# Kernel tuning notes

Hardware: AMD Instinct MI355X
Metric: run time of the kernel (lower is better)

Reference implementation:

```python
import jax, jax.numpy as jnp
import numpy as np

B, S, L, E, H, T, V, D = 32, 256, 24, 300, 256, 16, 50000, 256  # batch, sents, words/sent, emb, gru_units, topics, vocab, dense


def setup_inputs() -> dict:
    key = jax.random.key(0)
    ks = jax.random.split(key, 12)
    word_ids = jax.random.randint(ks[0], (B, S, L), 0, V, dtype=jnp.int32)
    tsize = S // T
    starts = (jnp.arange(T, dtype=jnp.int32) * tsize + 1)          # 1-indexed inclusive
    ends = (jnp.arange(T, dtype=jnp.int32) * tsize + tsize)
    topic_start_ends = jnp.broadcast_to(jnp.stack([starts, ends], -1)[None], (B, T, 2))
    g = lambda k, shape, sc=0.05: (jax.random.normal(k, shape, jnp.float32) * sc)
    return {
        "word_ids": word_ids,
        "topic_start_ends": topic_start_ends,
        "emb": g(ks[1], (V, E), 0.1),
        "Wih_f": g(ks[2], (3 * H, E)), "Whh_f": g(ks[3], (3 * H, H)),
        "bih_f": jnp.zeros((3 * H,), jnp.float32), "bhh_f": jnp.zeros((3 * H,), jnp.float32),
        "Wih_b": g(ks[4], (3 * H, E)), "Whh_b": g(ks[5], (3 * H, H)),
        "bih_b": jnp.zeros((3 * H,), jnp.float32), "bhh_b": jnp.zeros((3 * H,), jnp.float32),
        "W_att": g(ks[6], (4 * H, 4 * H)), "v_att": g(ks[7], (4 * H, 1)),
        "W_dna": g(ks[8], (4 * H, D)), "b_dna": jnp.zeros((D,), jnp.float32),
        "W_out": g(ks[9], (D, 1)), "b_out": jnp.zeros((1,), jnp.float32),
    }


def _gru_dir(x, Wih, Whh, bih, bhh, reverse):
    # x: [B, S, E] -> outputs [B, S, H], final hidden [B, H]  (PyTorch GRU cell math)
    def step(h, xt):
        gi = xt @ Wih.T + bih
        gh = h @ Whh.T + bhh
        ir, iz, inn = jnp.split(gi, 3, axis=-1)
        hr, hz, hn = jnp.split(gh, 3, axis=-1)
        r = jax.nn.sigmoid(ir + hr)
        z = jax.nn.sigmoid(iz + hz)
        n = jnp.tanh(inn + r * hn)
        h2 = (1.0 - z) * n + z * h
        return h2, h2
    h0 = jnp.zeros((x.shape[0], Whh.shape[1]), x.dtype)
    hT, ys = jax.lax.scan(step, h0, jnp.swapaxes(x, 0, 1), reverse=reverse)
    return jnp.swapaxes(ys, 0, 1), hT


def _gather_seq(x, idx):
    # x: [B, S', C], idx: [B, K] -> [B, K, C]
    return jnp.take_along_axis(x, idx[:, :, None].astype(jnp.int32), axis=1)


def reference(word_ids, topic_start_ends, emb, Wih_f, Whh_f, bih_f, bhh_f,
              Wih_b, Whh_b, bih_b, bhh_b, W_att, v_att, W_dna, b_dna, W_out, b_out):
    # --- sent_encoder: per-sentence mean of word embeddings ---
    sent_vecs = jnp.mean(emb[word_ids], axis=2)  # [B, S, E]

    # --- doc_encoder: bidirectional GRU ---
    out_f, hT_f = _gru_dir(sent_vecs, Wih_f, Whh_f, bih_f, bhh_f, reverse=False)
    out_b, hT_b = _gru_dir(sent_vecs, Wih_b, Whh_b, bih_b, bhh_b, reverse=True)
    sent_rep = jnp.concatenate([out_f, out_b], axis=-1)          # [B, S, 2H]
    hidden = jnp.stack([hT_f, hT_b], axis=0)                     # [2, B, H]
    # faithful to torch: hidden.view(batch_size, 2H) (row-major reshape)
    doc_vec = hidden.reshape(B, 2 * H)
    doc_rep = jnp.broadcast_to(doc_vec[:, None, :], (B, S, 2 * H))

    # --- topic representation via boundary differencing on front/back-padded output ---
    padded = jnp.pad(sent_rep, ((0, 0), (1, 1), (0, 0)))         # [B, S+2, 2H]
    starts = topic_start_ends[..., 0]                            # [B, T], 1-indexed
    ends = topic_start_ends[..., 1]
    topic_fwd = _gather_seq(padded, ends)[..., :H] - _gather_seq(padded, starts - 1)[..., :H]
    topic_bwd = _gather_seq(padded, starts)[..., H:] - _gather_seq(padded, ends + 1)[..., H:]
    topic_mat = jnp.concatenate([topic_fwd, topic_bwd], axis=-1)  # [B, T, 2H]
    # sentence s (0-indexed) -> topic t with starts[t] <= s+1 <= ends[t]
    sent_1idx = jnp.arange(1, S + 1, dtype=jnp.int32)
    topic_id = jax.vmap(lambda e: jnp.searchsorted(e, sent_1idx, side='left'))(ends)  # [B, S]
    topic_rep = jnp.take_along_axis(topic_mat, topic_id[:, :, None], axis=1)          # [B, S, 2H]

    # --- decoder_attention ---
    cat_ds = jnp.concatenate([doc_rep, sent_rep], axis=-1)       # [B, S, 4H]
    cat_ts = jnp.concatenate([topic_rep, sent_rep], axis=-1)
    doc_scores = jnp.tanh(cat_ds @ W_att) @ v_att                # [B, S, 1]
    topic_scores = jnp.tanh(cat_ts @ W_att) @ v_att
    doc_w = jax.nn.softmax(doc_scores, axis=1)
    topic_w = jax.nn.softmax(topic_scores, axis=1)
    context = doc_w * doc_rep + topic_w * topic_rep              # [B, S, 2H]
    inp = jnp.concatenate([sent_rep, context], axis=-1)          # [B, S, 4H]
    h = jax.nn.relu(inp @ W_dna + b_dna)                         # dropout is identity (eval)
    logits = (h @ W_out + b_out)[..., 0]                         # [B, S]
    return logits
```

## Files before the change

### kernel.cpp

```cpp
#include <hip/hip_runtime.h>
#include <hip/hip_bf16.h>
#include <math.h>

#define Bd 32
#define Sd 256
#define Ld 24
#define Ed 300
#define Hd 256
#define Td 16
#define Dd 256
#define EP 320

using short8 = __attribute__((ext_vector_type(8))) short;
using f32x4  = __attribute__((ext_vector_type(4))) float;

__device__ __forceinline__ float fsigm(float x) { return 1.f / (1.f + __expf(-x)); }
__device__ __forceinline__ float ftanh(float x) {
  float e = __expf(2.f * x);
  return 1.f - 2.f / (e + 1.f);
}

__global__ void sent_means_kernel(const int* __restrict__ wids,
                                  const float* __restrict__ emb,
                                  __hip_bfloat16* __restrict__ apad) {
  int r = blockIdx.x;
  __shared__ int ids[Ld];
  int tid = threadIdx.x;
  if (tid < Ld) ids[tid] = wids[r * Ld + tid];
  __syncthreads();
  float acc = 0.f;
  if (tid < Ed) {
#pragma unroll
    for (int w = 0; w < Ld; ++w) acc += emb[(size_t)ids[w] * Ed + tid];
    acc *= (1.f / 24.f);
  }
  apad[r * EP + tid] = __float2bfloat16(tid < Ed ? acc : 0.f);
}

__global__ void pad_wih_kernel(const float* __restrict__ src,
                               __hip_bfloat16* __restrict__ dst) {
  int i = blockIdx.x * 256 + threadIdx.x;
  if (i >= 768 * EP) return;
  int n = i / EP, k = i % EP;
  dst[i] = __float2bfloat16(k < Ed ? src[n * Ed + k] : 0.f);
}
__global__ void f2bf_kernel(const float* __restrict__ src,
                            __hip_bfloat16* __restrict__ dst, int n) {
  int i = blockIdx.x * 256 + threadIdx.x;
  if (i < n) dst[i] = __float2bfloat16(src[i]);
}
__global__ void transpose_att_kernel(const float* __restrict__ src,
                                     __hip_bfloat16* __restrict__ dst) {
  int i = blockIdx.x * 256 + threadIdx.x;
  int n = i >> 10, k = i & 1023;
  dst[i] = __float2bfloat16(src[k * 1024 + n]);
}
__global__ void transpose_dna_kernel(const float* __restrict__ src,
                                     __hip_bfloat16* __restrict__ dst) {
  int i = blockIdx.x * 256 + threadIdx.x;
  int n = i >> 10, k = i & 1023;
  dst[i] = __float2bfloat16(src[k * Dd + n]);
}

__global__ __launch_bounds__(256) void gemm_xwt_kernel(
    const __hip_bfloat16* __restrict__ A, int lda,
    const __hip_bfloat16* __restrict__ W, int ldw,
    float* __restrict__ C, int ldc,
    int M, int N, int K,
    const float* __restrict__ bias) {
  __shared__ unsigned short la[64][32];
  __shared__ unsigned short lb[64][32];
  const int tid = threadIdx.x;
  const int m0 = blockIdx.x * 64, n0 = blockIdx.y * 64;
  const int lane = tid & 63, wid = tid >> 6;
  const int wm = (wid >> 1) * 32, wn = (wid & 1) * 32;
  const int lrow = tid >> 2, lcol = (tid & 3) * 8;
  f32x4 acc00 = {0.f, 0.f, 0.f, 0.f}, acc01 = {0.f, 0.f, 0.f, 0.f};
  f32x4 acc10 = {0.f, 0.f, 0.f, 0.f}, acc11 = {0.f, 0.f, 0.f, 0.f};
  int arow = m0 + lrow; if (arow > M - 1) arow = M - 1;
  const int brow = n0 + lrow;
  const int fr = lane & 15, fq = (lane >> 4) * 8;
  for (int k0 = 0; k0 < K; k0 += 32) {
    uint4 av = *(const uint4*)(A + (size_t)arow * lda + k0 + lcol);
    uint4 bv = *(const uint4*)(W + (size_t)brow * ldw + k0 + lcol);
    *(uint4*)(&la[lrow][lcol]) = av;
    *(uint4*)(&lb[lrow][lcol]) = bv;
    __syncthreads();
    short8 a0 = *(const short8*)(&la[wm + fr][fq]);
    short8 a1 = *(const short8*)(&la[wm + 16 + fr][fq]);
    short8 b0 = *(const short8*)(&lb[wn + fr][fq]);
    short8 b1 = *(const short8*)(&lb[wn + 16 + fr][fq]);
    acc00 = __builtin_amdgcn_mfma_f32_16x16x32_bf16(a0, b0, acc00, 0, 0, 0);
    acc01 = __builtin_amdgcn_mfma_f32_16x16x32_bf16(a0, b1, acc01, 0, 0, 0);
    acc10 = __builtin_amdgcn_mfma_f32_16x16x32_bf16(a1, b0, acc10, 0, 0, 0);
    acc11 = __builtin_amdgcn_mfma_f32_16x16x32_bf16(a1, b1, acc11, 0, 0, 0);
    __syncthreads();
  }
  const int rq = (lane >> 4) * 4;
  f32x4 accs[2][2] = {{acc00, acc01}, {acc10, acc11}};
  for (int i = 0; i < 2; ++i)
    for (int j = 0; j < 2; ++j) {
      int n = n0 + wn + j * 16 + fr;
      float bv = bias ? bias[n] : 0.f;
      for (int r2 = 0; r2 < 4; ++r2) {
        int m = m0 + wm + i * 16 + rq + r2;
        if (m < M) C[(size_t)m * ldc + n] = accs[i][j][r2] + bv;
      }
    }
}

__global__ __launch_bounds__(512, 2) void gru_mfma_kernel(
    const float* __restrict__ gi_f, const float* __restrict__ gi_b,
    const __hip_bfloat16* __restrict__ whhbf_f, const __hip_bfloat16* __restrict__ whhbf_b,
    const float* __restrict__ bhh_f, const float* __restrict__ bhh_b,
    float* __restrict__ sent_rep, __hip_bfloat16* __restrict__ sent_rep_bf,
    float* __restrict__ hT_f, float* __restrict__ hT_b) {
  __shared__ float gi_lds[2][8][768];
  __shared__ __hip_bfloat16 h_bf[256];
  __shared__ float gh[768];
  __shared__ float stg32[8][256];
  const int blk = blockIdx.x;
  const int dir = blk >> 5, b = blk & 31;
  const int tid = threadIdx.x;
  const int lane = tid & 63, w = tid >> 6;
  const float* gi = dir ? gi_b : gi_f;
  const __hip_bfloat16* whh = dir ? whhbf_b : whhbf_f;
  const float* bhh = dir ? bhh_b : bhh_f;

  if (tid < 256) h_bf[tid] = __float2bfloat16(0.f);

  short8 bfrag[6][8];
  {
    const int n0 = w * 96 + (lane & 15);
    const int kq = (lane >> 4) * 8;
#pragma unroll
    for (int nt = 0; nt < 6; ++nt)
#pragma unroll
      for (int kt = 0; kt < 8; ++kt)
        bfrag[nt][kt] = *(const short8*)(whh + (size_t)(n0 + nt * 16) * 256 + kt * 32 + kq);
  }
  float bhr = 0.f, bhz = 0.f, bhn = 0.f, hprev = 0.f;
  if (tid < 256) { bhr = bhh[tid]; bhz = bhh[256 + tid]; bhn = bhh[512 + tid]; }

  auto burst = [&](int tstart, int buf) {
#pragma unroll
    for (int i = 0; i < 3; ++i) {
      int idx = tid + i * 512;
      int u = idx / 192;
      int c4 = (idx - u * 192) * 4;
      int s = dir ? (255 - (tstart + u)) : (tstart + u);
      float4 v = *(const float4*)(gi + (size_t)(((b << 8) + s) * 768 + c4));
      *(float4*)(&gi_lds[buf][u][c4]) = v;
    }
  };
  burst(0, 0);
  __syncthreads();

  const int c = lane & 15;
  const int kq = (lane >> 4) * 8;
  const short8 zero8 = {0, 0, 0, 0, 0, 0, 0, 0};

  for (int t = 0; t < Sd; ++t) {
    if ((t & 7) == 0 && t + 8 < Sd) burst(t + 8, ((t >> 3) + 1) & 1);
    f32x4 acc[6];
#pragma unroll
    for (int nt = 0; nt < 6; ++nt) acc[nt] = (f32x4){0.f, 0.f, 0.f, 0.f};
#pragma unroll
    for (int kt = 0; kt < 8; ++kt) {
      short8 av = *(const short8*)(&h_bf[kt * 32 + kq]);
      if (c != 0) av = zero8;
#pragma unroll
      for (int nt = 0; nt < 6; ++nt)
        acc[nt] = __builtin_amdgcn_mfma_f32_16x16x32_bf16(av, bfrag[nt][kt], acc[nt], 0, 0, 0);
    }
    if (lane < 16) {
#pragma unroll
      for (int nt = 0; nt < 6; ++nt)
        gh[w * 96 + nt * 16 + lane] = acc[nt][0];
    }
    __syncthreads();
    if (tid < 256) {
      const float* gl = gi_lds[(t >> 3) & 1][t & 7];
      float rr = fsigm(gl[tid] + gh[tid] + bhr);
      float zz = fsigm(gl[256 + tid] + gh[256 + tid] + bhz);
      float nn = ftanh(gl[512 + tid] + rr * (gh[512 + tid] + bhn));
      float hn = (1.f - zz) * nn + zz * hprev;
      hprev = hn;
      h_bf[tid] = __float2bfloat16(hn);
      stg32[t & 7][tid] = hn;
    }
    __syncthreads();
    if ((t & 7) == 7) {
      const int base = t - 7;
#pragma unroll
      for (int i = 0; i < 4; ++i) {
        int idx = tid + i * 512;
        int u = idx >> 8, d = idx & 255;
        int sg = dir ? (255 - (base + u)) : (base + u);
        size_t rowg = (size_t)((b << 8) + sg);
        int col = dir ? (256 + d) : d;
        float v = stg32[u][d];
        sent_rep[rowg * 512 + col] = v;
        sent_rep_bf[rowg * 512 + col] = __float2bfloat16(v);
      }
    }
  }
  if (tid < 256) (dir ? hT_b : hT_f)[b * 256 + tid] = hprev;
}

__global__ void docvec_kernel(const float* __restrict__ hTf, const float* __restrict__ hTb,
                              __hip_bfloat16* __restrict__ dv) {
  int b = blockIdx.x, jj = threadIdx.x;
  int idx = b * 512 + jj;
  int dsel = idx >> 13;
  int rem = idx & 8191;
  int bp = rem >> 8, hp = rem & 255;
  float v = (dsel ? hTb : hTf)[bp * Hd + hp];
  dv[idx] = __float2bfloat16(v);
}

__global__ void topic_kernel(const int* __restrict__ tse, const float* __restrict__ sent_rep,
                             __hip_bfloat16* __restrict__ topic_bf) {
  int bt = blockIdx.x;
  int b = bt >> 4;
  int st = tse[bt * 2], en = tse[bt * 2 + 1];
  int dd = threadIdx.x;
  auto pad = [&](int i, int col) -> float {
    if (i < 1 || i > Sd) return 0.f;
    return sent_rep[((size_t)((b << 8) + (i - 1))) * 512 + col];
  };
  float fwd = pad(en, dd) - pad(st - 1, dd);
  float bwd = pad(st, Hd + dd) - pad(en + 1, Hd + dd);
  topic_bf[(size_t)bt * 512 + dd] = __float2bfloat16(fwd);
  topic_bf[(size_t)bt * 512 + Hd + dd] = __float2bfloat16(bwd);
}

__global__ void scores_kernel(const float* __restrict__ P, const float* __restrict__ R,
                              const float* __restrict__ Q, const float* __restrict__ v_att,
                              const int* __restrict__ tse,
                              float* __restrict__ dsc, float* __restrict__ tsc) {
  int r = blockIdx.x;
  int b = r >> 8, s = r & 255;
  int tid = threadIdx.x;
  int tsel = Td - 1;
  for (int t = 0; t < Td; ++t) {
    if (tse[(b * Td + t) * 2 + 1] >= s + 1) { tsel = t; break; }
  }
  const float* q = Q + (size_t)r * 1024;
  const float* p = P + (size_t)b * 1024;
  const float* rr = R + (size_t)(b * Td + tsel) * 1024;
  float accd = 0.f, acct = 0.f;
  for (int n = tid; n < 1024; n += 256) {
    float qv = q[n];
    float vv = v_att[n];
    accd += ftanh(p[n] + qv) * vv;
    acct += ftanh(rr[n] + qv) * vv;
  }
  __shared__ float s1[256], s2[256];
  s1[tid] = accd; s2[tid] = acct;
  __syncthreads();
  for (int off = 128; off > 0; off >>= 1) {
    if (tid < off) { s1[tid] += s1[tid + off]; s2[tid] += s2[tid + off]; }
    __syncthreads();
  }
  if (tid == 0) { dsc[r] = s1[0]; tsc[r] = s2[0]; }
}

__global__ void softmax_kernel(const float* __restrict__ dsc, const float* __restrict__ tsc,
                               float* __restrict__ dw, float* __restrict__ tw) {
  int b = blockIdx.x, s = threadIdx.x;
  __shared__ float red[256];
  for (int which = 0; which < 2; ++which) {
    const float* src = which ? tsc : dsc;
    float v = src[b * Sd + s];
    red[s] = v; __syncthreads();
    for (int off = 128; off > 0; off >>= 1) {
      if (s < off) red[s] = fmaxf(red[s], red[s + off]);
      __syncthreads();
    }
    float m = red[0]; __syncthreads();
    float e = __expf(v - m);
    red[s] = e; __syncthreads();
    for (int off = 128; off > 0; off >>= 1) {
      if (s < off) red[s] += red[s + off];
      __syncthreads();
    }
    float sum = red[0]; __syncthreads();
    (which ? tw : dw)[b * Sd + s] = e / sum;
  }
}

__global__ void final_kernel(const float* __restrict__ U, const float* __restrict__ dvd,
                             const float* __restrict__ tvd, const float* __restrict__ dw,
                             const float* __restrict__ tw, const float* __restrict__ b_dna,
                             const float* __restrict__ w_out,
                             const float* __restrict__ b_out,
                             const int* __restrict__ tse, float* __restrict__ out) {
  int r = blockIdx.x;
  int b = r >> 8, s = r & 255;
  int dd = threadIdx.x;
  int tsel = Td - 1;
  for (int t = 0; t < Td; ++t) {
    if (tse[(b * Td + t) * 2 + 1] >= s + 1) { tsel = t; break; }
  }
  float wdv = dw[b * Sd + s], wtv = tw[b * Sd + s];
  float x = U[(size_t)r * Dd + dd] + wdv * dvd[b * Dd + dd] +
            wtv * tvd[(size_t)(b * Td + tsel) * Dd + dd] + b_dna[dd];
  x = fmaxf(x, 0.f);
  float term = x * w_out[dd];
  __shared__ float red[256];
  red[dd] = term; __syncthreads();
  for (int off = 128; off > 0; off >>= 1) {
    if (dd < off) red[dd] += red[dd + off];
    __syncthreads();
  }
  if (dd == 0) out[r] = red[0] + b_out[0];
}

static void launch_gemm(const __hip_bfloat16* A, int lda, const __hip_bfloat16* W, int ldw,
                        float* C, int ldc, int M, int N, int K,
                        const float* bias, hipStream_t stream) {
  dim3 grid((M + 63) / 64, N / 64);
  gemm_xwt_kernel<<<grid, 256, 0, stream>>>(A, lda, W, ldw, C, ldc, M, N, K, bias);
}

extern "C" void kernel_launch(void* const* d_in, const int* in_sizes, int n_in,
                              void* d_out, int out_size, void* d_ws, size_t ws_size,
                              hipStream_t stream) {
  const int* word_ids = (const int*)d_in[0];
  const int* tse      = (const int*)d_in[1];
  const float* emb   = (const float*)d_in[2];
  const float* wih_f = (const float*)d_in[3];
  const float* whh_f = (const float*)d_in[4];
  const float* bih_f = (const float*)d_in[5];
  const float* bhh_f = (const float*)d_in[6];
  const float* wih_b = (const float*)d_in[7];
  const float* whh_b = (const float*)d_in[8];
  const float* bih_b = (const float*)d_in[9];
  const float* bhh_b = (const float*)d_in[10];
  const float* w_att = (const float*)d_in[11];
  const float* v_att = (const float*)d_in[12];
  const float* w_dna = (const float*)d_in[13];
  const float* b_dna = (const float*)d_in[14];
  const float* w_out = (const float*)d_in[15];
  const float* b_out = (const float*)d_in[16];
  float* out = (float*)d_out;
  char* ws = (char*)d_ws;

  const int M = Bd * Sd;

  size_t off = 0;
  auto alloc = [&](size_t sz) { size_t o = off; off += (sz + 255) & ~(size_t)255; return o; };
  size_t o_svbf   = alloc((size_t)M * EP * 2);
  size_t o_wpadf  = alloc((size_t)768 * EP * 2);
  size_t o_wpadb  = alloc((size_t)768 * EP * 2);
  size_t o_whhbf  = alloc((size_t)768 * Hd * 2 * 2);
  size_t o_wattT  = alloc((size_t)1024 * 1024 * 2);
  size_t o_wdnaT  = alloc((size_t)Dd * 1024 * 2);
  size_t o_hTf    = alloc((size_t)Bd * Hd * 4);
  size_t o_hTb    = alloc((size_t)Bd * Hd * 4);
  size_t o_dvbf   = alloc((size_t)Bd * 512 * 2);
  size_t o_topbf  = alloc((size_t)Bd * Td * 512 * 2);
  size_t o_P      = alloc((size_t)Bd * 1024 * 4);
  size_t o_R      = alloc((size_t)Bd * Td * 1024 * 4);
  size_t o_dvd    = alloc((size_t)Bd * Dd * 4);
  size_t o_tvd    = alloc((size_t)Bd * Td * Dd * 4);
  size_t o_dsc    = alloc((size_t)Bd * Sd * 4);
  size_t o_tsc    = alloc((size_t)Bd * Sd * 4);
  size_t o_dw     = alloc((size_t)Bd * Sd * 4);
  size_t o_tw     = alloc((size_t)Bd * Sd * 4);
  size_t o_srep32 = alloc((size_t)M * 512 * 4);
  size_t o_srepbf = alloc((size_t)M * 512 * 2);
  size_t o_gif    = alloc((size_t)M * 768 * 4);
  size_t o_gib    = alloc((size_t)M * 768 * 4);
  size_t o_Q = o_gif;
  size_t o_U = o_gif + (size_t)M * 1024 * 4;
  (void)ws_size;

  __hip_bfloat16* svbf   = (__hip_bfloat16*)(ws + o_svbf);
  __hip_bfloat16* wpadf  = (__hip_bfloat16*)(ws + o_wpadf);
  __hip_bfloat16* wpadb  = (__hip_bfloat16*)(ws + o_wpadb);
  __hip_bfloat16* whhbf_f = (__hip_bfloat16*)(ws + o_whhbf);
  __hip_bfloat16* whhbf_b = whhbf_f + 768 * Hd;
  __hip_bfloat16* wattT  = (__hip_bfloat16*)(ws + o_wattT);
  __hip_bfloat16* wdnaT  = (__hip_bfloat16*)(ws + o_wdnaT);
  float* hTf = (float*)(ws + o_hTf);
  float* hTb = (float*)(ws + o_hTb);
  __hip_bfloat16* dvbf  = (__hip_bfloat16*)(ws + o_dvbf);
  __hip_bfloat16* topbf = (__hip_bfloat16*)(ws + o_topbf);
  float* P   = (float*)(ws + o_P);
  float* R   = (float*)(ws + o_R);
  float* dvd = (float*)(ws + o_dvd);
  float* tvd = (float*)(ws + o_tvd);
  float* dsc = (float*)(ws + o_dsc);
  float* tsc = (float*)(ws + o_tsc);
  float* dw  = (float*)(ws + o_dw);
  float* tw  = (float*)(ws + o_tw);
  float* srep32 = (float*)(ws + o_srep32);
  __hip_bfloat16* srepbf = (__hip_bfloat16*)(ws + o_srepbf);
  float* gif = (float*)(ws + o_gif);
  float* gib = (float*)(ws + o_gib);
  float* Q = (float*)(ws + o_Q);
  float* U = (float*)(ws + o_U);

  sent_means_kernel<<<M, EP, 0, stream>>>(word_ids, emb, svbf);
  pad_wih_kernel<<<(768 * EP) / 256, 256, 0, stream>>>(wih_f, wpadf);
  pad_wih_kernel<<<(768 * EP) / 256, 256, 0, stream>>>(wih_b, wpadb);
  f2bf_kernel<<<(768 * Hd) / 256, 256, 0, stream>>>(whh_f, whhbf_f, 768 * Hd);
  f2bf_kernel<<<(768 * Hd) / 256, 256, 0, stream>>>(whh_b, whhbf_b, 768 * Hd);
  transpose_att_kernel<<<(1024 * 1024) / 256, 256, 0, stream>>>(w_att, wattT);
  transpose_dna_kernel<<<(Dd * 1024) / 256, 256, 0, stream>>>(w_dna, wdnaT);
  launch_gemm(svbf, EP, wpadf, EP, gif, 768, M, 768, EP, bih_f, stream);
  launch_gemm(svbf, EP, wpadb, EP, gib, 768, M, 768, EP, bih_b, stream);
  gru_mfma_kernel<<<64, 512, 0, stream>>>(gif, gib, whhbf_f, whhbf_b, bhh_f, bhh_b,
                                          srep32, srepbf, hTf, hTb);
  docvec_kernel<<<Bd, 512, 0, stream>>>(hTf, hTb, dvbf);
  topic_kernel<<<Bd * Td, 256, 0, stream>>>(tse, srep32, topbf);
  launch_gemm(srepbf, 512, wattT + 512, 1024, Q, 1024, M, 1024, 512, nullptr, stream);
  launch_gemm(dvbf, 512, wattT, 1024, P, 1024, Bd, 1024, 512, nullptr, stream);
  launch_gemm(topbf, 512, wattT, 1024, R, 1024, Bd * Td, 1024, 512, nullptr, stream);
  launch_gemm(srepbf, 512, wdnaT, 1024, U, Dd, M, Dd, 512, nullptr, stream);
  launch_gemm(dvbf, 512, wdnaT + 512, 1024, dvd, Dd, Bd, Dd, 512, nullptr, stream);
  launch_gemm(topbf, 512, wdnaT + 512, 1024, tvd, Dd, Bd * Td, Dd, 512, nullptr, stream);
  scores_kernel<<<M, 256, 0, stream>>>(P, R, Q, v_att, tse, dsc, tsc);
  softmax_kernel<<<Bd, 256, 0, stream>>>(dsc, tsc, dw, tw);
  final_kernel<<<M, 256, 0, stream>>>(U, dvd, tvd, dw, tw, b_dna, w_out, b_out, tse, out);
}
```

Before: 623.3 us.

## Pack attention and dense weights, merge GEMMs, overlap weight prep with GRU

Merges the four weight-conversion kernels for the GRU into a single prep kernel. The W_att and W_dna transposes move into extra blocks of the GRU kernel so they run alongside the latency-bound recurrence. W_att and W_dna are packed into two 1280x512 bf16 matrices, so the six projection GEMMs become three with N=1280, and the scores and final kernels read the new combined layouts. This removes several launches and the separate transpose pass, at the cost of a strided transpose inside the GRU launch that may compete with the recurrence blocks.

```diff
diff --git a/kernel.cpp b/kernel.cpp
--- a/kernel.cpp
+++ b/kernel.cpp
@@ -37,29 +37,26 @@
   apad[r * EP + tid] = __float2bfloat16(tid < Ed ? acc : 0.f);
 }
 
-__global__ void pad_wih_kernel(const float* __restrict__ src,
-                               __hip_bfloat16* __restrict__ dst) {
-  int i = blockIdx.x * 256 + threadIdx.x;
-  if (i >= 768 * EP) return;
-  int n = i / EP, k = i % EP;
-  dst[i] = __float2bfloat16(k < Ed ? src[n * Ed + k] : 0.f);
-}
-__global__ void f2bf_kernel(const float* __restrict__ src,
-                            __hip_bfloat16* __restrict__ dst, int n) {
-  int i = blockIdx.x * 256 + threadIdx.x;
-  if (i < n) dst[i] = __float2bfloat16(src[i]);
-}
-__global__ void transpose_att_kernel(const float* __restrict__ src,
-                                     __hip_bfloat16* __restrict__ dst) {
-  int i = blockIdx.x * 256 + threadIdx.x;
-  int n = i >> 10, k = i & 1023;
-  dst[i] = __float2bfloat16(src[k * 1024 + n]);
-}
-__global__ void transpose_dna_kernel(const float* __restrict__ src,
-                                     __hip_bfloat16* __restrict__ dst) {
-  int i = blockIdx.x * 256 + threadIdx.x;
-  int n = i >> 10, k = i & 1023;
-  dst[i] = __float2bfloat16(src[k * Dd + n]);
+__global__ void prep1_kernel(const float* __restrict__ wih_f, const float* __restrict__ wih_b,
+                             const float* __restrict__ whh_f, const float* __restrict__ whh_b,
+                             __hip_bfloat16* __restrict__ wpadf, __hip_bfloat16* __restrict__ wpadb,
+                             __hip_bfloat16* __restrict__ whhbf_f, __hip_bfloat16* __restrict__ whhbf_b) {
+  int i = blockIdx.x * 512 + threadIdx.x;
+  const int PW = 768 * EP;
+  const int WH = 768 * Hd;
+  if (i < 2 * PW) {
+    const float* src = (i < PW) ? wih_f : wih_b;
+    __hip_bfloat16* dst = (i < PW) ? wpadf : wpadb;
+    int j = (i < PW) ? i : i - PW;
+    int n = j / EP, k = j % EP;
+    dst[j] = __float2bfloat16(k < Ed ? src[n * Ed + k] : 0.f);
+  } else {
+    int j = i - 2 * PW;
+    const float* src = (j < WH) ? whh_f : whh_b;
+    __hip_bfloat16* dst = (j < WH) ? whhbf_f : whhbf_b;
+    int k = (j < WH) ? j : j - WH;
+    dst[k] = __float2bfloat16(src[k]);
+  }
 }
 
 __global__ __launch_bounds__(256) void gemm_xwt_kernel(
@@ -114,14 +111,40 @@
     const __hip_bfloat16* __restrict__ whhbf_f, const __hip_bfloat16* __restrict__ whhbf_b,
     const float* __restrict__ bhh_f, const float* __restrict__ bhh_b,
     float* __restrict__ sent_rep, __hip_bfloat16* __restrict__ sent_rep_bf,
-    float* __restrict__ hT_f, float* __restrict__ hT_b) {
+    float* __restrict__ hT_f, float* __restrict__ hT_b,
+    const float* __restrict__ w_att, const float* __restrict__ w_dna,
+    __hip_bfloat16* __restrict__ wpack1, __hip_bfloat16* __restrict__ wpack2) {
   __shared__ float gi_lds[2][8][768];
   __shared__ __hip_bfloat16 h_bf[256];
   __shared__ float gh[768];
   __shared__ float stg32[8][256];
   const int blk = blockIdx.x;
+  const int tid = threadIdx.x;
+
+  if (blk >= 64) {
+    const size_t q = (size_t)(blk - 64) * 512 + tid;
+    size_t flat = q * 8;
+    const size_t HALF = (size_t)1280 * 512;
+    const bool second = flat >= HALF;
+    size_t r = second ? flat - HALF : flat;
+    int n = (int)(r >> 9), k0 = (int)(r & 511);
+    __hip_bfloat16* dst = second ? wpack2 : wpack1;
+#pragma unroll
+    for (int j = 0; j < 8; ++j) {
+      int k = k0 + j;
+      float v;
+      if (!second)
+        v = (n < 1024) ? w_att[(size_t)k * 1024 + n]
+                       : w_dna[(size_t)(512 + k) * 256 + (n - 1024)];
+      else
+        v = (n < 1024) ? w_att[(size_t)(512 + k) * 1024 + n]
+                       : w_dna[(size_t)k * 256 + (n - 1024)];
+      dst[(size_t)n * 512 + k] = __float2bfloat16(v);
+    }
+    return;
+  }
+
   const int dir = blk >> 5, b = blk & 31;
-  const int tid = threadIdx.x;
   const int lane = tid & 63, w = tid >> 6;
   const float* gi = dir ? gi_b : gi_f;
   const __hip_bfloat16* whh = dir ? whhbf_b : whhbf_f;
@@ -235,8 +258,8 @@
   topic_bf[(size_t)bt * 512 + Hd + dd] = __float2bfloat16(bwd);
 }
 
-__global__ void scores_kernel(const float* __restrict__ P, const float* __restrict__ R,
-                              const float* __restrict__ Q, const float* __restrict__ v_att,
+__global__ void scores_kernel(const float* __restrict__ PD, const float* __restrict__ RT,
+                              const float* __restrict__ QU, const float* __restrict__ v_att,
                               const int* __restrict__ tse,
                               float* __restrict__ dsc, float* __restrict__ tsc) {
   int r = blockIdx.x;
@@ -246,9 +269,9 @@
   for (int t = 0; t < Td; ++t) {
     if (tse[(b * Td + t) * 2 + 1] >= s + 1) { tsel = t; break; }
   }
-  const float* q = Q + (size_t)r * 1024;
-  const float* p = P + (size_t)b * 1024;
-  const float* rr = R + (size_t)(b * Td + tsel) * 1024;
+  const float* q = QU + (size_t)r * 1280;
+  const float* p = PD + (size_t)b * 1280;
+  const float* rr = RT + (size_t)(b * Td + tsel) * 1280;
   float accd = 0.f, acct = 0.f;
   for (int n = tid; n < 1024; n += 256) {
     float qv = q[n];
@@ -290,8 +313,8 @@
   }
 }
 
-__global__ void final_kernel(const float* __restrict__ U, const float* __restrict__ dvd,
-                             const float* __restrict__ tvd, const float* __restrict__ dw,
+__global__ void final_kernel(const float* __restrict__ QU, const float* __restrict__ PD,
+                             const float* __restrict__ RT, const float* __restrict__ dw,
                              const float* __restrict__ tw, const float* __restrict__ b_dna,
                              const float* __restrict__ w_out,
                              const float* __restrict__ b_out,
@@ -304,8 +327,8 @@
     if (tse[(b * Td + t) * 2 + 1] >= s + 1) { tsel = t; break; }
   }
   float wdv = dw[b * Sd + s], wtv = tw[b * Sd + s];
-  float x = U[(size_t)r * Dd + dd] + wdv * dvd[b * Dd + dd] +
-            wtv * tvd[(size_t)(b * Td + tsel) * Dd + dd] + b_dna[dd];
+  float x = QU[(size_t)r * 1280 + 1024 + dd] + wdv * PD[(size_t)b * 1280 + 1024 + dd] +
+            wtv * RT[(size_t)(b * Td + tsel) * 1280 + 1024 + dd] + b_dna[dd];
   x = fmaxf(x, 0.f);
   float term = x * w_out[dd];
   __shared__ float red[256];
@@ -355,16 +378,14 @@
   size_t o_wpadf  = alloc((size_t)768 * EP * 2);
   size_t o_wpadb  = alloc((size_t)768 * EP * 2);
   size_t o_whhbf  = alloc((size_t)768 * Hd * 2 * 2);
-  size_t o_wattT  = alloc((size_t)1024 * 1024 * 2);
-  size_t o_wdnaT  = alloc((size_t)Dd * 1024 * 2);
+  size_t o_wpack1 = alloc((size_t)1280 * 512 * 2);
+  size_t o_wpack2 = alloc((size_t)1280 * 512 * 2);
   size_t o_hTf    = alloc((size_t)Bd * Hd * 4);
   size_t o_hTb    = alloc((size_t)Bd * Hd * 4);
   size_t o_dvbf   = alloc((size_t)Bd * 512 * 2);
   size_t o_topbf  = alloc((size_t)Bd * Td * 512 * 2);
-  size_t o_P      = alloc((size_t)Bd * 1024 * 4);
-  size_t o_R      = alloc((size_t)Bd * Td * 1024 * 4);
-  size_t o_dvd    = alloc((size_t)Bd * Dd * 4);
-  size_t o_tvd    = alloc((size_t)Bd * Td * Dd * 4);
+  size_t o_PD     = alloc((size_t)Bd * 1280 * 4);
+  size_t o_RT     = alloc((size_t)Bd * Td * 1280 * 4);
   size_t o_dsc    = alloc((size_t)Bd * Sd * 4);
   size_t o_tsc    = alloc((size_t)Bd * Sd * 4);
   size_t o_dw     = alloc((size_t)Bd * Sd * 4);
@@ -373,8 +394,7 @@
   size_t o_srepbf = alloc((size_t)M * 512 * 2);
   size_t o_gif    = alloc((size_t)M * 768 * 4);
   size_t o_gib    = alloc((size_t)M * 768 * 4);
-  size_t o_Q = o_gif;
-  size_t o_U = o_gif + (size_t)M * 1024 * 4;
+  size_t o_QU = o_gif;
   (void)ws_size;
 
   __hip_bfloat16* svbf   = (__hip_bfloat16*)(ws + o_svbf);
@@ -382,16 +402,14 @@
   __hip_bfloat16* wpadb  = (__hip_bfloat16*)(ws + o_wpadb);
   __hip_bfloat16* whhbf_f = (__hip_bfloat16*)(ws + o_whhbf);
   __hip_bfloat16* whhbf_b = whhbf_f + 768 * Hd;
-  __hip_bfloat16* wattT  = (__hip_bfloat16*)(ws + o_wattT);
-  __hip_bfloat16* wdnaT  = (__hip_bfloat16*)(ws + o_wdnaT);
+  __hip_bfloat16* wpack1 = (__hip_bfloat16*)(ws + o_wpack1);
+  __hip_bfloat16* wpack2 = (__hip_bfloat16*)(ws + o_wpack2);
   float* hTf = (float*)(ws + o_hTf);
   float* hTb = (float*)(ws + o_hTb);
   __hip_bfloat16* dvbf  = (__hip_bfloat16*)(ws + o_dvbf);
   __hip_bfloat16* topbf = (__hip_bfloat16*)(ws + o_topbf);
-  float* P   = (float*)(ws + o_P);
-  float* R   = (float*)(ws + o_R);
-  float* dvd = (float*)(ws + o_dvd);
-  float* tvd = (float*)(ws + o_tvd);
+  float* PD  = (float*)(ws + o_PD);
+  float* RT  = (float*)(ws + o_RT);
   float* dsc = (float*)(ws + o_dsc);
   float* tsc = (float*)(ws + o_tsc);
   float* dw  = (float*)(ws + o_dw);
@@ -400,29 +418,22 @@
   __hip_bfloat16* srepbf = (__hip_bfloat16*)(ws + o_srepbf);
   float* gif = (float*)(ws + o_gif);
   float* gib = (float*)(ws + o_gib);
-  float* Q = (float*)(ws + o_Q);
-  float* U = (float*)(ws + o_U);
+  float* QU  = (float*)(ws + o_QU);
 
   sent_means_kernel<<<M, EP, 0, stream>>>(word_ids, emb, svbf);
-  pad_wih_kernel<<<(768 * EP) / 256, 256, 0, stream>>>(wih_f, wpadf);
-  pad_wih_kernel<<<(768 * EP) / 256, 256, 0, stream>>>(wih_b, wpadb);
-  f2bf_kernel<<<(768 * Hd) / 256, 256, 0, stream>>>(whh_f, whhbf_f, 768 * Hd);
-  f2bf_kernel<<<(768 * Hd) / 256, 256, 0, stream>>>(whh_b, whhbf_b, 768 * Hd);
-  transpose_att_kernel<<<(1024 * 1024) / 256, 256, 0, stream>>>(w_att, wattT);
-  transpose_dna_kernel<<<(Dd * 1024) / 256, 256, 0, stream>>>(w_dna, wdnaT);
+  prep1_kernel<<<1728, 512, 0, stream>>>(wih_f, wih_b, whh_f, whh_b,
+                                         wpadf, wpadb, whhbf_f, whhbf_b);
   launch_gemm(svbf, EP, wpadf, EP, gif, 768, M, 768, EP, bih_f, stream);
   launch_gemm(svbf, EP, wpadb, EP, gib, 768, M, 768, EP, bih_b, stream);
-  gru_mfma_kernel<<<64, 512, 0, stream>>>(gif, gib, whhbf_f, whhbf_b, bhh_f, bhh_b,
-                                          srep32, srepbf, hTf, hTb);
+  gru_mfma_kernel<<<384, 512, 0, stream>>>(gif, gib, whhbf_f, whhbf_b, bhh_f, bhh_b,
+                                           srep32, srepbf, hTf, hTb,
+                                           w_att, w_dna, wpack1, wpack2);
   docvec_kernel<<<Bd, 512, 0, stream>>>(hTf, hTb, dvbf);
   topic_kernel<<<Bd * Td, 256, 0, stream>>>(tse, srep32, topbf);
-  launch_gemm(srepbf, 512, wattT + 512, 1024, Q, 1024, M, 1024, 512, nullptr, stream);
-  launch_gemm(dvbf, 512, wattT, 1024, P, 1024, Bd, 1024, 512, nullptr, stream);
-  launch_gemm(topbf, 512, wattT, 1024, R, 1024, Bd * Td, 1024, 512, nullptr, stream);
-  launch_gemm(srepbf, 512, wdnaT, 1024, U, Dd, M, Dd, 512, nullptr, stream);
-  launch_gemm(dvbf, 512, wdnaT + 512, 1024, dvd, Dd, Bd, Dd, 512, nullptr, stream);
-  launch_gemm(topbf, 512, wdnaT + 512, 1024, tvd, Dd, Bd * Td, Dd, 512, nullptr, stream);
-  scores_kernel<<<M, 256, 0, stream>>>(P, R, Q, v_att, tse, dsc, tsc);
+  launch_gemm(srepbf, 512, wpack2, 512, QU, 1280, M, 1280, 512, nullptr, stream);
+  launch_gemm(dvbf, 512, wpack1, 512, PD, 1280, Bd, 1280, 512, nullptr, stream);
+  launch_gemm(topbf, 512, wpack1, 512, RT, 1280, Bd * Td, 1280, 512, nullptr, stream);
+  scores_kernel<<<M, 256, 0, stream>>>(PD, RT, QU, v_att, tse, dsc, tsc);
   softmax_kernel<<<Bd, 256, 0, stream>>>(dsc, tsc, dw, tw);
-  final_kernel<<<M, 256, 0, stream>>>(U, dvd, tvd, dw, tw, b_dna, w_out, b_out, tse, out);
-}
+  final_kernel<<<M, 256, 0, stream>>>(QU, PD, RT, dw, tw, b_dna, w_out, b_out, tse, out);
+}
```

After: 582.0 us. 1.07x faster.
